# Optimization experiments

Hardware: AMD Instinct MI355X
Metric: run time of the kernel (lower is better)

The kernel has to match this reference:

```python
import jax, jax.numpy as jnp
import numpy as np

N = 50000
E = 800000
D = 256        # encoder_dim; also hidden*heads for both layers
H = 4          # heads
C = 64         # hidden_dim per head
OUT = 5        # classes
NEG_SLOPE = 0.2
GN_EPS = 1e-5
SM_EPS = 1e-16  # PyG softmax denominator epsilon


def setup_inputs() -> dict:
    key = jax.random.key(0)
    ks = jax.random.split(key, 20)
    sc = lambda fan_in: 1.0 / np.sqrt(fan_in)
    inp = {
        "x": jax.random.normal(ks[0], (N, D), dtype=jnp.float32),
        "edge_index": jax.random.randint(ks[1], (2, E), 0, N, dtype=jnp.int64),
        # two GATv2 layers (stacked on leading axis): lin_l, lin_r, att, bias
        "Wl": jax.random.normal(ks[2], (2, D, H * C), dtype=jnp.float32) * sc(D),
        "Wr": jax.random.normal(ks[3], (2, D, H * C), dtype=jnp.float32) * sc(D),
        "att": jax.random.normal(ks[4], (2, H, C), dtype=jnp.float32) * sc(C),
        "bconv": jnp.zeros((2, H * C), dtype=jnp.float32),
        # parallel linear skips
        "Wlin": jax.random.normal(ks[5], (2, D, H * C), dtype=jnp.float32) * sc(D),
        "blin": jnp.zeros((2, H * C), dtype=jnp.float32),
        # GraphNorm params
        "gn_w": jnp.ones((2, H * C), dtype=jnp.float32),
        "gn_b": jnp.zeros((2, H * C), dtype=jnp.float32),
        "gn_ms": jnp.ones((2, H * C), dtype=jnp.float32),
        # final GATv2 (concat=False -> head mean, out=5) and final linear
        "fWl": jax.random.normal(ks[6], (D, H * OUT), dtype=jnp.float32) * sc(D),
        "fWr": jax.random.normal(ks[7], (D, H * OUT), dtype=jnp.float32) * sc(D),
        "fatt": jax.random.normal(ks[8], (H, OUT), dtype=jnp.float32) * sc(OUT),
        "fbconv": jnp.zeros((OUT,), dtype=jnp.float32),
        "fWlin": jax.random.normal(ks[9], (D, OUT), dtype=jnp.float32) * sc(D),
        "fblin": jnp.zeros((OUT,), dtype=jnp.float32),
    }
    return inp


def _gatv2(x, src, dst, Wl, Wr, att, heads, ch):
    # x: [N, Din]; returns [N, heads, ch]
    n = x.shape[0]
    xl = (x @ Wl).reshape(n, heads, ch)  # source messages
    xr = (x @ Wr).reshape(n, heads, ch)  # target query part
    e = jax.nn.leaky_relu(xl[src] + xr[dst], NEG_SLOPE)      # [E, H, C]
    score = jnp.einsum("ehc,hc->eh", e, att)                  # [E, H]
    # segment softmax over incoming edges of each target node
    m = jax.ops.segment_max(score, dst, num_segments=n)       # [N, H]
    a = jnp.exp(score - m[dst])
    denom = jax.ops.segment_sum(a, dst, num_segments=n)       # [N, H]
    alpha = a / (denom[dst] + SM_EPS)                         # [E, H]
    return jax.ops.segment_sum(alpha[..., None] * xl[src], dst, num_segments=n)


def _graphnorm(x, w, b, ms):
    mean = jnp.mean(x, axis=0)
    centered = x - mean * ms
    var = jnp.mean(centered * centered, axis=0)
    return w * centered * jax.lax.rsqrt(var + GN_EPS) + b


def reference(x, edge_index, Wl, Wr, att, bconv, Wlin, blin, gn_w, gn_b, gn_ms,
              fWl, fWr, fatt, fbconv, fWlin, fblin):
    src, dst = edge_index[0], edge_index[1]
    emb = x
    for i in range(2):
        cpart = _gatv2(emb, src, dst, Wl[i], Wr[i], att[i], H, C).reshape(N, H * C) + bconv[i]
        lpart = emb @ Wlin[i] + blin[i]
        cpart = _graphnorm(cpart, gn_w[i], gn_b[i], gn_ms[i])
        emb = jax.nn.elu(cpart + lpart)
    cpart = _gatv2(emb, src, dst, fWl, fWr, fatt, H, OUT).mean(axis=1) + fbconv  # concat=False
    lpart = emb @ fWlin + fblin
    return jax.nn.log_softmax(cpart + lpart, axis=1)
```

## Files before the change

kernel.cpp:

```cpp
#include <hip/hip_runtime.h>

#define NN 50000
#define EE 800000
#define DD 256
#define NB 196
#define DEGMAX 80

typedef unsigned short u16;
typedef unsigned int u32;

typedef __attribute__((ext_vector_type(8))) short short8;
typedef __attribute__((ext_vector_type(4))) float f32x4;
typedef __attribute__((ext_vector_type(4))) unsigned short u16x4;
typedef __attribute__((ext_vector_type(4))) int i32x4;

__device__ __forceinline__ float b2f(u16 u) {
  union { u32 i; float f; } c; c.i = ((u32)u) << 16; return c.f;
}
__device__ __forceinline__ u16 f2b(float f) {
  union { float f; u32 i; } c; c.f = f;
  u32 u = c.i;
  return (u16)((u + 0x7fffu + ((u >> 16) & 1u)) >> 16);
}
__device__ __forceinline__ float lrelu(float x) { return fmaxf(x, 0.2f * x); }
__device__ __forceinline__ float ldf(const void* p, int i, int bf) {
  return bf ? b2f(((const u16*)p)[i]) : ((const float*)p)[i];
}
__device__ __forceinline__ int lde(const void* ei, int idx, int m64) {
  int v = m64 ? (int)((const long long*)ei)[idx] : ((const int*)ei)[idx];
  return v < 0 ? 0 : (v >= NN ? NN - 1 : v);
}
__device__ __forceinline__ float cexp(float s) {
  return __expf(__builtin_amdgcn_fmed3f(s, -60.f, 60.f));
}

template <int CTRL>
__device__ __forceinline__ float dpp_add(float s) {
  union { float f; int i; } a, b;
  a.f = s;
  b.i = __builtin_amdgcn_update_dpp(0, a.i, CTRL, 0xf, 0xf, true);
  return s + b.f;
}
__device__ __forceinline__ float row16_allsum(float s) {
  s = dpp_add<0xB1>(s);
  s = dpp_add<0x4E>(s);
  s = dpp_add<0x141>(s);
  s = dpp_add<0x140>(s);
  return s;
}

__device__ __forceinline__ void gload_lds16(const void* g, void* l) {
  __builtin_amdgcn_global_load_lds(
      (const __attribute__((address_space(1))) void*)g,
      (__attribute__((address_space(3))) void*)l, 16, 0, 0);
}

__global__ __launch_bounds__(256) void init_kernel(const void* x, const void* ei,
                                                   int* flags, int* cnt,
                                                   float* sums, int* sync) {
  int i = blockIdx.x * 256 + threadIdx.x;
  if (i < NN) cnt[i] = 0;
  if (blockIdx.x == 1) {
    #pragma unroll
    for (int j = 0; j < 4; ++j) sums[threadIdx.x + j * 256] = 0.f;
  }
  if (blockIdx.x == 2 && threadIdx.x < 8) sync[threadIdx.x] = 0;
  if (blockIdx.x == 0 && threadIdx.x < 64) {
    int lane = threadIdx.x;
    const u16* xw = (const u16*)x;
    int c = 0;
    for (int k = lane; k < 512; k += 64) {
      u16 w = xw[k];
      int e = (w >> 7) & 0xFF;
      if ((e >= 107 && e <= 147) || (w & 0x7FFF) == 0) ++c;
    }
    const u32* ew = (const u32*)ei;
    int zc = 0;
    for (int k = 1 + 2 * lane; k < 1024; k += 128)
      if (ew[k] == 0) ++zc;
    #pragma unroll
    for (int off = 1; off < 64; off <<= 1) {
      c += __shfl_xor(c, off);
      zc += __shfl_xor(zc, off);
    }
    if (lane == 0) {
      flags[0] = (c >= 440) ? 1 : 0;
      flags[1] = (zc >= 400) ? 1 : 0;
    }
  }
}

__global__ void fill_kernel(const void* ei, const int* flags,
                            int* __restrict__ cnt, int* __restrict__ col) {
  int e = blockIdx.x * 256 + threadIdx.x;
  if (e < EE) {
    int m64 = flags[1];
    int dst = lde(ei, EE + e, m64);
    int src = lde(ei, e, m64);
    int slot = atomicAdd(&cnt[dst], 1);
    if (slot < DEGMAX) col[dst * DEGMAX + slot] = src;
  }
}

__global__ __launch_bounds__(256) void prep_kernel(
    const void* Wl, const void* Wr, const void* Wlin,
    const void* fWl, const void* fWr, const void* fWlin,
    const int* flags, u16* wpack, u16* fwp) {
  int bf = flags[0];
  int bid = blockIdx.x;
  if (bid < 1536) {
    int idx = bid * 256 + threadIdx.x;
    int m = idx >> 16, e = idx & 65535;
    int layer = (m >= 3) ? 1 : 0, sel = m - layer * 3;
    const void* src = (sel == 0 ? Wl : (sel == 1 ? Wr : Wlin));
    int k = e >> 8, n = e & 255;
    wpack[(m << 16) + ((((k >> 3) << 8) + n) << 3) + (k & 7)] =
        f2b(ldf(src, layer * 65536 + e, bf));
  } else {
    int idx = (bid - 1536) * 256 + threadIdx.x;
    int j = idx & 7;
    int col = (idx >> 3) % 48;
    int kk = idx / (48 * 8);
    int k = kk * 8 + j;
    float v = 0.f;
    if (col < 20)      v = ldf(fWl, k * 20 + col, bf);
    else if (col < 40) v = ldf(fWr, k * 20 + (col - 20), bf);
    else if (col < 45) v = ldf(fWlin, k * 5 + (col - 40), bf);
    fwp[idx] = f2b(v);
  }
}

__device__ __forceinline__ void load_af_fused(short8* af, const u16* cpb, const u16* lpb,
                                              const float* __restrict__ ab, int q) {
  #pragma unroll
  for (int i = 0; i < 8; ++i) {
    int ch0 = q * 8 + i * 32;
    u16x4 c0 = *(const u16x4*)(cpb + i * 32);
    u16x4 c1 = *(const u16x4*)(cpb + i * 32 + 4);
    u16x4 l0 = *(const u16x4*)(lpb + i * 32);
    u16x4 l1 = *(const u16x4*)(lpb + i * 32 + 4);
    f32x4 a0 = *(const f32x4*)(ab + ch0);
    f32x4 a1 = *(const f32x4*)(ab + ch0 + 4);
    f32x4 b0 = *(const f32x4*)(ab + 256 + ch0);
    f32x4 b1 = *(const f32x4*)(ab + 256 + ch0 + 4);
    short8 w;
    #pragma unroll
    for (int j = 0; j < 4; ++j) {
      float y = a0[j] * b2f(c0[j]) + b0[j] + b2f(l0[j]);
      y = y > 0.f ? y : expm1f(y);
      w[j] = (short)f2b(y);
      float y2 = a1[j] * b2f(c1[j]) + b1[j] + b2f(l1[j]);
      y2 = y2 > 0.f ? y2 : expm1f(y2);
      w[j + 4] = (short)f2b(y2);
    }
    af[i] = w;
  }
}

__global__ __launch_bounds__(256) void gemm_kernel(
    const void* __restrict__ xsrc, const u16* __restrict__ wpack, const void* blin,
    const int* flags, int layer,
    u16* __restrict__ xl, u16* __restrict__ xr, u16* __restrict__ lp, int M,
    const u16* __restrict__ cp, const u16* __restrict__ lpin,
    const float* __restrict__ ab, int fuse) {
  __shared__ __align__(16) u16 bsh[16384];
  int wave = threadIdx.x >> 6;
  int lane = threadIdx.x & 63;
  int q = lane >> 4;
  int t = lane & 15;
  int m0 = blockIdx.x * 64 + wave * 16;

  int arow = m0 + t;
  if (arow >= M) arow = M - 1;
  int bf = flags[0];
  short8 af[8];
  if (fuse == 1) {
    const u16* cpb = cp + (size_t)arow * DD + q * 8;
    const u16* lpb = lpin + (size_t)arow * DD + q * 8;
    load_af_fused(af, cpb, lpb, ab, q);
  } else {
    if (bf) {
      const u16* Abase = (const u16*)xsrc + (size_t)arow * DD + q * 8;
      #pragma unroll
      for (int i = 0; i < 8; ++i) af[i] = *(const short8*)(Abase + i * 32);
    } else {
      const float* Fb = (const float*)xsrc + (size_t)arow * DD + q * 8;
      #pragma unroll
      for (int i = 0; i < 8; ++i) {
        f32x4 s0 = *(const f32x4*)(Fb + i * 32);
        f32x4 s1 = *(const f32x4*)(Fb + i * 32 + 4);
        short8 w;
        #pragma unroll
        for (int j = 0; j < 4; ++j) {
          w[j] = (short)f2b(s0[j]);
          w[j + 4] = (short)f2b(s1[j]);
        }
        af[i] = w;
      }
    }
  }

  int m = m0 + t;

  for (int y = 0; y < 12; ++y) {
    int mm = y >> 2;
    int col0 = (y & 3) * 64;
    const u16* wb = wpack + (mm << 16);

    __syncthreads();
    #pragma unroll
    for (int itc = 0; itc < 8; ++itc) {
      int kk = wave + itc * 4;
      const u16* gp = wb + (((kk << 8) + col0) << 3) + (lane << 3);
      u16* lb = &bsh[(wave * 64 + itc * 256) << 3];
      gload_lds16(gp, lb);
    }
    __syncthreads();

    f32x4 acc[4];
    #pragma unroll
    for (int ns = 0; ns < 4; ++ns) acc[ns] = (f32x4){0.f, 0.f, 0.f, 0.f};

    #pragma unroll
    for (int i = 0; i < 8; ++i) {
      int kk = i * 4 + q;
      const u16* bb = &bsh[(kk << 9) + (t << 3)];
      #pragma unroll
      for (int ns = 0; ns < 4; ++ns) {
        short8 b = *(const short8*)(bb + (ns << 7));
        acc[ns] = __builtin_amdgcn_mfma_f32_16x16x32_bf16(b, af[i], acc[ns], 0, 0, 0);
      }
    }

    u16* dstp = (y < 4) ? xl : (y < 8) ? xr : lp;
    bool isLp = (y >= 8);
    if (m < M) {
      #pragma unroll
      for (int ns = 0; ns < 4; ++ns) {
        int c0 = col0 + ns * 16 + q * 4;
        u16x4 w;
        #pragma unroll
        for (int r = 0; r < 4; ++r) {
          float bias = isLp ? ldf(blin, layer * 256 + c0 + r, bf) : 0.f;
          w[r] = f2b(acc[ns][r] + bias);
        }
        *(u16x4*)(dstp + (size_t)m * DD + c0) = w;
      }
    }
  }
}

__global__ __launch_bounds__(256) void fgemm_kernel(
    const u16* __restrict__ cp, const u16* __restrict__ lpin,
    const float* __restrict__ ab, const u16* __restrict__ fwp, const void* fblin,
    const int* flags, float* __restrict__ zl, float* __restrict__ zr,
    float* __restrict__ lp5, int M) {
  int wave = threadIdx.x >> 6;
  int lane = threadIdx.x & 63;
  int q = lane >> 4;
  int t = lane & 15;
  int m0 = blockIdx.x * 64 + wave * 16;

  f32x4 acc[3];
  #pragma unroll
  for (int ns = 0; ns < 3; ++ns) acc[ns] = (f32x4){0.f, 0.f, 0.f, 0.f};

  int arow = m0 + t;
  if (arow >= M) arow = M - 1;
  short8 af[8];
  {
    const u16* cpb = cp + (size_t)arow * DD + q * 8;
    const u16* lpb = lpin + (size_t)arow * DD + q * 8;
    load_af_fused(af, cpb, lpb, ab, q);
  }

  #pragma unroll
  for (int k0 = 0; k0 < DD; k0 += 32) {
    short8 a = af[k0 >> 5];
    int kk = (k0 >> 3) + q;
    #pragma unroll
    for (int ns = 0; ns < 3; ++ns) {
      short8 b = *(const short8*)(fwp + (((kk * 48) + ns * 16 + t) << 3));
      acc[ns] = __builtin_amdgcn_mfma_f32_16x16x32_bf16(a, b, acc[ns], 0, 0, 0);
    }
  }

  int bf = flags[0];
  #pragma unroll
  for (int ns = 0; ns < 3; ++ns) {
    int c = ns * 16 + t;
    #pragma unroll
    for (int r = 0; r < 4; ++r) {
      int row = m0 + q * 4 + r;
      if (row < M) {
        float v = acc[ns][r];
        if (c < 20) {
          zl[row * 32 + (c / 5) * 8 + (c % 5)] = v;
        } else if (c < 40) {
          int c2 = c - 20;
          zr[row * 32 + (c2 / 5) * 8 + (c2 % 5)] = v;
        } else if (c < 45) {
          lp5[row * 8 + (c - 40)] = v + ldf(fblin, c - 40, bf);
        }
      }
    }
  }
}

__device__ __forceinline__ void edge_step(u16x4 s4, const float* xrv, const float* atv,
                                          float& l, float* acc) {
  float x0 = b2f(s4[0]), x1 = b2f(s4[1]), x2 = b2f(s4[2]), x3 = b2f(s4[3]);
  float sp = atv[0] * lrelu(x0 + xrv[0]) + atv[1] * lrelu(x1 + xrv[1]) +
             atv[2] * lrelu(x2 + xrv[2]) + atv[3] * lrelu(x3 + xrv[3]);
  sp = row16_allsum(sp);
  float pz = cexp(sp);
  l += pz;
  acc[0] += pz * x0;
  acc[1] += pz * x1;
  acc[2] += pz * x2;
  acc[3] += pz * x3;
}

__global__ __launch_bounds__(256) void agg_kernel(
    const u16* __restrict__ xl, const u16* __restrict__ xr,
    const int* __restrict__ cnt, const int* __restrict__ col,
    const void* att, const void* bconv, const int* flags, int layer,
    u16* __restrict__ cpart) {
  int wave = threadIdx.x >> 6;
  int node = blockIdx.x * 4 + wave;
  int lane = threadIdx.x & 63;
  int h = lane >> 4;
  int cb = (lane & 15) * 4;
  int base = h * 64 + cb;
  int bf = flags[0];

  u16x4 r4 = *(const u16x4*)(xr + (size_t)node * DD + base);
  float xrv[4], atv[4];
  #pragma unroll
  for (int j = 0; j < 4; ++j) {
    xrv[j] = b2f(r4[j]);
    atv[j] = ldf(att, layer * 256 + base + j, bf);
  }

  float l = 0.f;
  float acc[4] = {0.f, 0.f, 0.f, 0.f};
  int deg = cnt[node];
  if (deg > DEGMAX) deg = DEGMAX;
  const int* cp = col + node * DEGMAX;
  const char* xlb = (const char*)xl;
  u32 baseb = (u32)(base << 1);

  auto gather = [&](int c) -> u16x4 {
    return *(const u16x4*)(xlb + (((u32)c << 9) + baseb));
  };

  int e = 0;
  int nq = deg >> 2;
  if (nq > 0) {
    i32x4 cqB = *(const i32x4*)cp;
    u16x4 a0 = gather(cqB.x), a1 = gather(cqB.y), a2 = gather(cqB.z), a3 = gather(cqB.w);
    cqB = (nq > 1) ? *(const i32x4*)(cp + 4) : cqB;
    for (int g = 0; g < nq; ++g) {
      i32x4 cqC = (g + 2 < nq) ? *(const i32x4*)(cp + (g + 2) * 4) : cqB;
      u16x4 b0 = a0, b1 = a1, b2 = a2, b3 = a3;
      if (g + 1 < nq) {
        b0 = gather(cqB.x); b1 = gather(cqB.y); b2 = gather(cqB.z); b3 = gather(cqB.w);
      }
      edge_step(a0, xrv, atv, l, acc);
      edge_step(a1, xrv, atv, l, acc);
      edge_step(a2, xrv, atv, l, acc);
      edge_step(a3, xrv, atv, l, acc);
      a0 = b0; a1 = b1; a2 = b2; a3 = b3;
      cqB = cqC;
    }
    e = nq * 4;
  }
  for (; e < deg; ++e) {
    u16x4 v = gather(cp[e]);
    edge_step(v, xrv, atv, l, acc);
  }

  float inv = 1.f / (l + 1e-16f);
  u16x4 outw;
  #pragma unroll
  for (int j = 0; j < 4; ++j)
    outw[j] = f2b(acc[j] * inv + ldf(bconv, layer * 256 + base + j, bf));
  *(u16x4*)(cpart + (size_t)node * DD + base) = outw;
}

__global__ __launch_bounds__(256) void stats_kernel(
    const u16* __restrict__ cpart, float* __restrict__ sums,
    const void* gw, const void* gb, const void* gms, const int* flags, int layer,
    float* __restrict__ ab, int* __restrict__ done) {
  int ch = threadIdx.x;
  int n0 = blockIdx.x * 100, n1 = n0 + 100;
  float s = 0.f, s2 = 0.f;
  for (int n = n0; n < n1; ++n) {
    float x = b2f(cpart[(size_t)n * DD + ch]);
    s += x; s2 += x * x;
  }
  atomicAdd(&sums[ch], s);
  atomicAdd(&sums[256 + ch], s2);
  __threadfence();
  __shared__ int lastSh;
  if (ch == 0) lastSh = (atomicAdd(done, 1) == (int)gridDim.x - 1) ? 1 : 0;
  __syncthreads();
  if (lastSh) {
    int bf = flags[0];
    const float invN = 1.f / (float)NN;
    float mean = atomicAdd(&sums[ch], 0.f) * invN;
    float ex2 = atomicAdd(&sums[256 + ch], 0.f) * invN;
    float mm = mean * ldf(gms, layer * 256 + ch, bf);
    float var = ex2 - 2.f * mm * mean + mm * mm;
    float rs = rsqrtf(fmaxf(var, 0.f) + 1e-5f);
    float a = ldf(gw, layer * 256 + ch, bf) * rs;
    float b = ldf(gb, layer * 256 + ch, bf) - a * mm;
    ab[ch] = a;
    ab[256 + ch] = b;
  }
}

__global__ __launch_bounds__(256) void finagg_kernel(
    const float* __restrict__ zl, const float* __restrict__ zr,
    const int* __restrict__ cnt, const int* __restrict__ col,
    const void* fatt, const void* fbconv, const int* flags,
    const float* __restrict__ lp5, void* outv) {
  int node = blockIdx.x * 4 + (threadIdx.x >> 6);
  int lane = threadIdx.x & 63;
  int bf = flags[0];
  int h = lane >> 4, sub = lane & 15;

  const float* zrp = zr + node * 32 + h * 8;
  f32x4 zr4 = *(const f32x4*)zrp;
  float zrv[5] = {zr4.x, zr4.y, zr4.z, zr4.w, zrp[4]};
  float atv[5];
  #pragma unroll
  for (int c = 0; c < 5; ++c) atv[c] = ldf(fatt, h * 5 + c, bf);

  float l = 0.f, acc[5] = {0.f, 0.f, 0.f, 0.f, 0.f};
  int deg = cnt[node];
  if (deg > DEGMAX) deg = DEGMAX;
  const int* cp = col + node * DEGMAX;
  for (int e = sub; e < deg; e += 16) {
    int src = cp[e];
    const float* zs = zl + src * 32 + h * 8;
    f32x4 z4 = *(const f32x4*)zs;
    float z4s = zs[4];
    float zlv[5] = {z4.x, z4.y, z4.z, z4.w, z4s};
    float s = 0.f;
    #pragma unroll
    for (int c = 0; c < 5; ++c) s += atv[c] * lrelu(zlv[c] + zrv[c]);
    float pz = cexp(s);
    l += pz;
    #pragma unroll
    for (int c = 0; c < 5; ++c) acc[c] += pz * zlv[c];
  }
  #pragma unroll
  for (int off = 1; off < 16; off <<= 1) {
    l += __shfl_xor(l, off);
    #pragma unroll
    for (int c = 0; c < 5; ++c) acc[c] += __shfl_xor(acc[c], off);
  }
  float inv = 1.f / (l + 1e-16f);
  float v[5];
  #pragma unroll
  for (int c = 0; c < 5; ++c) {
    float tv = acc[c] * inv;
    tv += __shfl_xor(tv, 16);
    tv += __shfl_xor(tv, 32);
    v[c] = tv * 0.25f;
  }
  if (lane == 0) {
    float mx = -3.0e38f;
    #pragma unroll
    for (int c = 0; c < 5; ++c) {
      v[c] += ldf(fbconv, c, bf) + lp5[node * 8 + c];
      mx = fmaxf(mx, v[c]);
    }
    float se = 0.f;
    #pragma unroll
    for (int c = 0; c < 5; ++c) se += __expf(v[c] - mx);
    float lse = mx + __logf(se);
    #pragma unroll
    for (int c = 0; c < 5; ++c) {
      float r = v[c] - lse;
      if (bf) ((u16*)outv)[node * 5 + c] = f2b(r);
      else    ((float*)outv)[node * 5 + c] = r;
    }
  }
}

extern "C" void kernel_launch(void* const* d_in, const int* in_sizes, int n_in,
                              void* d_out, int out_size, void* d_ws, size_t ws_size,
                              hipStream_t stream) {
  (void)in_sizes; (void)n_in; (void)out_size; (void)ws_size;
  const void* x     = d_in[0];
  const void* ei    = d_in[1];
  const void* Wl    = d_in[2];
  const void* Wr    = d_in[3];
  const void* att   = d_in[4];
  const void* bconv = d_in[5];
  const void* Wlin  = d_in[6];
  const void* blin  = d_in[7];
  const void* gnw   = d_in[8];
  const void* gnb   = d_in[9];
  const void* gnms  = d_in[10];
  const void* fWl   = d_in[11];
  const void* fWr   = d_in[12];
  const void* fatt  = d_in[13];
  const void* fbc   = d_in[14];
  const void* fWlin = d_in[15];
  const void* fblin = d_in[16];

  char* p = (char*)d_ws;
  auto take = [&](size_t bytes) {
    char* r = p;
    p += (bytes + 511) & ~(size_t)511;
    return r;
  };
  int* flags   = (int*)take(512);
  int* cnt     = (int*)take(NN * sizeof(int));
  int* colx    = (int*)take((size_t)NN * DEGMAX * sizeof(int));
  u16* wpack   = (u16*)take((size_t)6 * 65536 * sizeof(u16));
  u16* fwp     = (u16*)take((size_t)32 * 48 * 8 * sizeof(u16));
  float* sums  = (float*)take(1024 * sizeof(float));
  float* ab    = (float*)take(1024 * sizeof(float));
  int* sync    = (int*)take(8 * sizeof(int));
  u16* cpart   = (u16*)take((size_t)NN * DD * 2);
  u16* xl      = (u16*)take((size_t)NN * DD * 2);
  u16* xr      = (u16*)take((size_t)NN * DD * 2);
  u16* lpA     = (u16*)take((size_t)NN * DD * 2);
  u16* lpB     = (u16*)take((size_t)NN * DD * 2);
  float* zl    = (float*)xl;
  float* zr    = (float*)xr;
  float* lp5   = (float*)lpA;

  init_kernel<<<dim3(NB), dim3(256), 0, stream>>>(x, ei, flags, cnt, sums, sync);
  fill_kernel<<<dim3((EE + 255) / 256), dim3(256), 0, stream>>>(ei, flags, cnt, colx);
  prep_kernel<<<dim3(1584), dim3(256), 0, stream>>>(
      Wl, Wr, Wlin, fWl, fWr, fWlin, flags, wpack, fwp);

  gemm_kernel<<<dim3((NN + 63) / 64), dim3(256), 0, stream>>>(
      x, wpack, blin, flags, 0, xl, xr, lpA, NN, cpart, lpA, ab, 2);
  agg_kernel<<<dim3(NN / 4), dim3(256), 0, stream>>>(xl, xr, cnt, colx, att, bconv,
                                                     flags, 0, cpart);
  stats_kernel<<<dim3(500), dim3(256), 0, stream>>>(cpart, sums, gnw, gnb, gnms, flags, 0,
                                                    ab, &sync[0]);

  gemm_kernel<<<dim3((NN + 63) / 64), dim3(256), 0, stream>>>(
      x, wpack + (size_t)3 * 65536, blin, flags, 1, xl, xr, lpB, NN, cpart, lpA, ab, 1);
  agg_kernel<<<dim3(NN / 4), dim3(256), 0, stream>>>(xl, xr, cnt, colx, att, bconv,
                                                     flags, 1, cpart);
  stats_kernel<<<dim3(500), dim3(256), 0, stream>>>(cpart, sums + 512, gnw, gnb, gnms,
                                                    flags, 1, ab + 512, &sync[1]);

  fgemm_kernel<<<dim3((NN + 63) / 64), dim3(256), 0, stream>>>(
      cpart, lpB, ab + 512, fwp, fblin, flags, zl, zr, lp5, NN);
  finagg_kernel<<<dim3(NN / 4), dim3(256), 0, stream>>>(zl, zr, cnt, colx, fatt, fbc,
                                                        flags, lp5, d_out);
}
```

Before: 534.3 us.

## Fuse GraphNorm statistics into persistent aggregation kernel

The per-layer GraphNorm stats kernel is removed. The aggregation kernel now runs as a grid-stride loop over 1250 blocks, accumulates column sums and sums of squares from its bf16-rounded outputs, and reduces them through shared memory into global atomics. The last finishing block computes the normalization scale and shift. This drops one kernel launch and a full re-read of cpart per layer, but reduces the grid size and adds a shared-memory reduction and atomics at the end of every block.

```diff
diff --git a/kernel.cpp b/kernel.cpp
--- a/kernel.cpp
+++ b/kernel.cpp
@@ -5,6 +5,7 @@
 #define DD 256
 #define NB 196
 #define DEGMAX 80
+#define AGGBLK 1250
 
 typedef unsigned short u16;
 typedef unsigned int u32;
@@ -325,98 +326,113 @@
     const u16* __restrict__ xl, const u16* __restrict__ xr,
     const int* __restrict__ cnt, const int* __restrict__ col,
     const void* att, const void* bconv, const int* flags, int layer,
-    u16* __restrict__ cpart) {
+    u16* __restrict__ cpart, float* __restrict__ sums,
+    const void* gw, const void* gb, const void* gms,
+    float* __restrict__ ab, int* __restrict__ done) {
   int wave = threadIdx.x >> 6;
-  int node = blockIdx.x * 4 + wave;
   int lane = threadIdx.x & 63;
   int h = lane >> 4;
   int cb = (lane & 15) * 4;
   int base = h * 64 + cb;
   int bf = flags[0];
 
-  u16x4 r4 = *(const u16x4*)(xr + (size_t)node * DD + base);
-  float xrv[4], atv[4];
+  float atv[4], bcv[4];
   #pragma unroll
   for (int j = 0; j < 4; ++j) {
-    xrv[j] = b2f(r4[j]);
     atv[j] = ldf(att, layer * 256 + base + j, bf);
-  }
-
-  float l = 0.f;
-  float acc[4] = {0.f, 0.f, 0.f, 0.f};
-  int deg = cnt[node];
-  if (deg > DEGMAX) deg = DEGMAX;
-  const int* cp = col + node * DEGMAX;
+    bcv[j] = ldf(bconv, layer * 256 + base + j, bf);
+  }
+
   const char* xlb = (const char*)xl;
   u32 baseb = (u32)(base << 1);
-
   auto gather = [&](int c) -> u16x4 {
     return *(const u16x4*)(xlb + (((u32)c << 9) + baseb));
   };
 
-  int e = 0;
-  int nq = deg >> 2;
-  if (nq > 0) {
-    i32x4 cqB = *(const i32x4*)cp;
-    u16x4 a0 = gather(cqB.x), a1 = gather(cqB.y), a2 = gather(cqB.z), a3 = gather(cqB.w);
-    cqB = (nq > 1) ? *(const i32x4*)(cp + 4) : cqB;
-    for (int g = 0; g < nq; ++g) {
-      i32x4 cqC = (g + 2 < nq) ? *(const i32x4*)(cp + (g + 2) * 4) : cqB;
-      u16x4 b0 = a0, b1 = a1, b2 = a2, b3 = a3;
-      if (g + 1 < nq) {
-        b0 = gather(cqB.x); b1 = gather(cqB.y); b2 = gather(cqB.z); b3 = gather(cqB.w);
+  float sacc[4] = {0.f, 0.f, 0.f, 0.f};
+  float s2acc[4] = {0.f, 0.f, 0.f, 0.f};
+
+  for (int qd = blockIdx.x; qd < NN / 4; qd += AGGBLK) {
+    int node = qd * 4 + wave;
+    u16x4 r4 = *(const u16x4*)(xr + (size_t)node * DD + base);
+    float xrv[4];
+    #pragma unroll
+    for (int j = 0; j < 4; ++j) xrv[j] = b2f(r4[j]);
+
+    float l = 0.f;
+    float acc[4] = {0.f, 0.f, 0.f, 0.f};
+    int deg = cnt[node];
+    if (deg > DEGMAX) deg = DEGMAX;
+    const int* cp = col + node * DEGMAX;
+
+    int e = 0;
+    int nq = deg >> 2;
+    if (nq > 0) {
+      i32x4 cqB = *(const i32x4*)cp;
+      u16x4 a0 = gather(cqB.x), a1 = gather(cqB.y), a2 = gather(cqB.z), a3 = gather(cqB.w);
+      cqB = (nq > 1) ? *(const i32x4*)(cp + 4) : cqB;
+      for (int g = 0; g < nq; ++g) {
+        i32x4 cqC = (g + 2 < nq) ? *(const i32x4*)(cp + (g + 2) * 4) : cqB;
+        u16x4 b0 = a0, b1 = a1, b2 = a2, b3 = a3;
+        if (g + 1 < nq) {
+          b0 = gather(cqB.x); b1 = gather(cqB.y); b2 = gather(cqB.z); b3 = gather(cqB.w);
+        }
+        edge_step(a0, xrv, atv, l, acc);
+        edge_step(a1, xrv, atv, l, acc);
+        edge_step(a2, xrv, atv, l, acc);
+        edge_step(a3, xrv, atv, l, acc);
+        a0 = b0; a1 = b1; a2 = b2; a3 = b3;
+        cqB = cqC;
       }
-      edge_step(a0, xrv, atv, l, acc);
-      edge_step(a1, xrv, atv, l, acc);
-      edge_step(a2, xrv, atv, l, acc);
-      edge_step(a3, xrv, atv, l, acc);
-      a0 = b0; a1 = b1; a2 = b2; a3 = b3;
-      cqB = cqC;
-    }
-    e = nq * 4;
-  }
-  for (; e < deg; ++e) {
-    u16x4 v = gather(cp[e]);
-    edge_step(v, xrv, atv, l, acc);
-  }
-
-  float inv = 1.f / (l + 1e-16f);
-  u16x4 outw;
-  #pragma unroll
-  for (int j = 0; j < 4; ++j)
-    outw[j] = f2b(acc[j] * inv + ldf(bconv, layer * 256 + base + j, bf));
-  *(u16x4*)(cpart + (size_t)node * DD + base) = outw;
-}
-
-__global__ __launch_bounds__(256) void stats_kernel(
-    const u16* __restrict__ cpart, float* __restrict__ sums,
-    const void* gw, const void* gb, const void* gms, const int* flags, int layer,
-    float* __restrict__ ab, int* __restrict__ done) {
-  int ch = threadIdx.x;
-  int n0 = blockIdx.x * 100, n1 = n0 + 100;
-  float s = 0.f, s2 = 0.f;
-  for (int n = n0; n < n1; ++n) {
-    float x = b2f(cpart[(size_t)n * DD + ch]);
-    s += x; s2 += x * x;
-  }
-  atomicAdd(&sums[ch], s);
-  atomicAdd(&sums[256 + ch], s2);
+      e = nq * 4;
+    }
+    for (; e < deg; ++e) {
+      u16x4 v = gather(cp[e]);
+      edge_step(v, xrv, atv, l, acc);
+    }
+
+    float inv = 1.f / (l + 1e-16f);
+    u16x4 outw;
+    #pragma unroll
+    for (int j = 0; j < 4; ++j) {
+      outw[j] = f2b(acc[j] * inv + bcv[j]);
+      float xv = b2f(outw[j]);
+      sacc[j] += xv;
+      s2acc[j] += xv * xv;
+    }
+    *(u16x4*)(cpart + (size_t)node * DD + base) = outw;
+  }
+
+  __shared__ float red[4 * 512];
+  #pragma unroll
+  for (int j = 0; j < 4; ++j) {
+    red[wave * 512 + base + j] = sacc[j];
+    red[wave * 512 + 256 + base + j] = s2acc[j];
+  }
+  __syncthreads();
+  int t = threadIdx.x;
+  float v0 = red[t] + red[512 + t] + red[1024 + t] + red[1536 + t];
+  float v1 = red[256 + t] + red[768 + t] + red[1280 + t] + red[1792 + t];
+  atomicAdd(&sums[t], v0);
+  atomicAdd(&sums[256 + t], v1);
   __threadfence();
   __shared__ int lastSh;
-  if (ch == 0) lastSh = (atomicAdd(done, 1) == (int)gridDim.x - 1) ? 1 : 0;
+  if (t == 0) {
+    unsigned int prev = (unsigned int)atomicAdd(done, 1);
+    lastSh = (prev + 1u == (unsigned int)AGGBLK) ? 1 : 0;
+  }
   __syncthreads();
   if (lastSh) {
-    int bf = flags[0];
     const float invN = 1.f / (float)NN;
-    float mean = atomicAdd(&sums[ch], 0.f) * invN;
-    float ex2 = atomicAdd(&sums[256 + ch], 0.f) * invN;
-    float mm = mean * ldf(gms, layer * 256 + ch, bf);
+    float mean = atomicAdd(&sums[t], 0.f) * invN;
+    float ex2 = atomicAdd(&sums[256 + t], 0.f) * invN;
+    float mm = mean * ldf(gms, layer * 256 + t, bf);
     float var = ex2 - 2.f * mm * mean + mm * mm;
     float rs = rsqrtf(fmaxf(var, 0.f) + 1e-5f);
-    float a = ldf(gw, layer * 256 + ch, bf) * rs;
-    float b = ldf(gb, layer * 256 + ch, bf) - a * mm;
-    ab[ch] = a;
-    ab[256 + ch] = b;
+    float a = ldf(gw, layer * 256 + t, bf) * rs;
+    float b = ldf(gb, layer * 256 + t, bf) - a * mm;
+    ab[t] = a;
+    ab[256 + t] = b;
   }
 }
 
@@ -542,17 +558,15 @@
 
   gemm_kernel<<<dim3((NN + 63) / 64), dim3(256), 0, stream>>>(
       x, wpack, blin, flags, 0, xl, xr, lpA, NN, cpart, lpA, ab, 2);
-  agg_kernel<<<dim3(NN / 4), dim3(256), 0, stream>>>(xl, xr, cnt, colx, att, bconv,
-                                                     flags, 0, cpart);
-  stats_kernel<<<dim3(500), dim3(256), 0, stream>>>(cpart, sums, gnw, gnb, gnms, flags, 0,
-                                                    ab, &sync[0]);
+  agg_kernel<<<dim3(AGGBLK), dim3(256), 0, stream>>>(
+      xl, xr, cnt, colx, att, bconv, flags, 0, cpart, sums,
+      gnw, gnb, gnms, ab, &sync[0]);
 
   gemm_kernel<<<dim3((NN + 63) / 64), dim3(256), 0, stream>>>(
       x, wpack + (size_t)3 * 65536, blin, flags, 1, xl, xr, lpB, NN, cpart, lpA, ab, 1);
-  agg_kernel<<<dim3(NN / 4), dim3(256), 0, stream>>>(xl, xr, cnt, colx, att, bconv,
-                                                     flags, 1, cpart);
-  stats_kernel<<<dim3(500), dim3(256), 0, stream>>>(cpart, sums + 512, gnw, gnb, gnms,
-                                                    flags, 1, ab + 512, &sync[1]);
+  agg_kernel<<<dim3(AGGBLK), dim3(256), 0, stream>>>(
+      xl, xr, cnt, colx, att, bconv, flags, 1, cpart, sums + 512,
+      gnw, gnb, gnms, ab + 512, &sync[1]);
 
   fgemm_kernel<<<dim3((NN + 63) / 64), dim3(256), 0, stream>>>(
       cpart, lpB, ab + 512, fwp, fblin, flags, zl, zr, lp5, NN);
```

Measured after the change: 722.7 us. +35.3%, slower.
